# Performance work log

Measured on AMD Instinct MI355X. Metric: run time of the kernel, lower is better.

## Reference

```python
import jax, jax.numpy as jnp
import numpy as np

B, T_Q, T_K, H = 16, 1024, 1024, 1024


def _linear_params(key, fan_in, fan_out):
    kw, kb = jax.random.split(key)
    bound = 1.0 / np.sqrt(fan_in)
    W = jax.random.uniform(kw, (fan_out, fan_in), jnp.float32, -bound, bound)
    b = jax.random.uniform(kb, (fan_out,), jnp.float32, -bound, bound)
    return W, b


def setup_inputs() -> dict:
    key = jax.random.key(0)
    ks = jax.random.split(key, 6)
    query = jax.random.normal(ks[0], (B, T_Q, H), jnp.float32)
    keys = jax.random.normal(ks[1], (B, T_K, H), jnp.float32)
    values = jax.random.normal(ks[2], (B, T_K, H), jnp.float32)
    Wq, bq = _linear_params(ks[3], H, H)
    Wk, bk = _linear_params(ks[4], H, H)
    Wo, bo = _linear_params(ks[5], H, H)
    return {"query": query, "keys": keys, "values": values,
            "Wq": Wq, "bq": bq, "Wk": Wk, "bk": bk, "Wo": Wo, "bo": bo}


def reference(query, keys, values, Wq, bq, Wk, bk, Wo, bo):
    # Linear projections (torch Linear: x @ W.T + b)
    q = jnp.einsum('bth,oh->bto', query, Wq) + bq   # (B, T_Q, H)
    k = jnp.einsum('bsh,oh->bso', keys, Wk) + bk    # (B, T_K, H)
    # Unscaled scores -> softmax over key axis (dropout is identity at eval)
    scores = jnp.einsum('bto,bso->bts', q, k)       # (B, T_Q, T_K)
    attn = jax.nn.softmax(scores, axis=-1)
    ctx = jnp.einsum('bts,bsh->bth', attn, values)  # note: raw values, value_fc unused in source
    ctx = ctx / jnp.sqrt(jnp.float32(values.shape[1]))
    out = jnp.einsum('bth,oh->bto', ctx, Wo) + bo
    return out
```

## Files before the change

kernel.cpp:

```cpp
#include <hip/hip_runtime.h>
#include <math.h>

typedef __attribute__((ext_vector_type(4))) float f32x4;
typedef __attribute__((ext_vector_type(8))) _Float16 h16x8;
typedef __attribute__((ext_vector_type(8))) short s16x8;
typedef __attribute__((ext_vector_type(4))) short s16x4;

__device__ inline unsigned short f2h(float f) {
    union { _Float16 h; unsigned short u; } v; v.h = (_Float16)f; return v.u;
}
__device__ inline float h2f(unsigned short u) {
    union { unsigned short u; _Float16 h; } v; v.u = u; return (float)v.h;
}

__device__ inline void async16(const void* g, void* l) {
    __builtin_amdgcn_global_load_lds(
        (const __attribute__((address_space(1))) unsigned int*)g,
        (__attribute__((address_space(3))) unsigned int*)l, 16, 0, 0);
}

#define BM 256
#define BN 256
#define BK 64
#define NTHREADS 512


__device__ inline void stage_half(const unsigned short* g, int row0, int kel, int pitch,
                                  unsigned ldsbase, char* smem, int tid) {
    const int rl  = tid >> 3;
    const int scb = ((tid & 7) ^ (rl & 7)) << 4;
    char* wb = smem + ldsbase + (unsigned)((tid >> 6) << 10);
#pragma unroll
    for (int s = 0; s < 2; ++s) {
        long off = ((long)(row0 + s * 64 + rl) * pitch + kel) * 2 + scb;
        async16((const char*)g + off, wb + s * 8192);
    }
}

__device__ inline h16x8 ld_frag(const char* smem, unsigned base, int row, int kbyte) {
    unsigned off = base + (unsigned)(row * 128) + (unsigned)(kbyte ^ ((row & 7) << 4));
    return *(const h16x8*)(smem + off);
}

__device__ inline void xcd_swizzle(int& bx, int& by, int& bz) {
    const long gx = gridDim.x, gy = gridDim.y;
    const long nwg = gx * gy * (long)gridDim.z;
    const long hw  = ((long)blockIdx.z * gy + blockIdx.y) * gx + blockIdx.x;
    const long qq = nwg >> 3, rr = nwg & 7;
    const long xcd = hw & 7, pos = hw >> 3;
    const long lg = (xcd < rr) ? xcd * (qq + 1) + pos
                               : rr * (qq + 1) + (xcd - rr) * qq + pos;
    bx = (int)(lg % gx);
    const long rem = lg / gx;
    by = (int)(rem % gy);
    bz = (int)(rem / gy);
}

template<int OM>
__global__ __launch_bounds__(NTHREADS, 2)
void gemm256(const unsigned short* __restrict__ A,
             const unsigned short* __restrict__ B,
             const float* __restrict__ bias,
             void* __restrict__ C, int N, int lenK, int pitch,
             long sA, long sB, long sC, long sBias, float scale)
{
    __shared__ __align__(16) char smem[131072];

    const int tid  = threadIdx.x;
    const int wv   = tid >> 6;
    const int lane = tid & 63;
    const int wr = wv >> 2, wc = wv & 3;
    const int lrow = lane & 15;
    const int kq16 = (lane >> 4) * 16;

    int bx, by, bz; xcd_swizzle(bx, by, bz);
    const int n0 = bx * BN;
    const int m0 = by * BM;

    const unsigned short* Ag = A + (long)bz * sA;
    const unsigned short* Bg = B + (long)bz * sB;
    const int NT = lenK / BK;

    auto stageA = [&](int t, int h) {
        stage_half(Ag, m0 + h * 128, t * BK, pitch,
                   (unsigned)(((t & 1) << 16) + (h << 14)), smem, tid);
    };
    auto stageB = [&](int t, int h) {
        stage_half(Bg, n0 + h * 128, t * BK, pitch,
                   (unsigned)(((t & 1) << 16) + 32768 + (h << 14)), smem, tid);
    };

    f32x4 acc[8][4];
#pragma unroll
    for (int i = 0; i < 8; ++i)
#pragma unroll
        for (int j = 0; j < 4; ++j) acc[i][j] = (f32x4){0.f, 0.f, 0.f, 0.f};

    const unsigned AbaseW = (unsigned)(wr * 16384);
    const unsigned BbaseW = (unsigned)(32768 + (wc >> 1) * 16384);
    const int brow0 = (wc & 1) * 64;

    stageB(0, 0); stageB(0, 1); stageA(0, 0); stageA(0, 1); stageB(1, 0); stageB(1, 1);
    asm volatile("s_waitcnt vmcnt(4)" ::: "memory");
    __builtin_amdgcn_s_barrier();

    h16x8 bfr[4][2], afr[2][2];

    for (int i = 0; i < NT / 2; ++i) {
        const int t1 = 2 * i + 1, t2 = 2 * i + 2, t3 = 2 * i + 3;
#pragma unroll
        for (int half = 0; half < 2; ++half) {
            const unsigned hb = half ? 65536u : 0u;
#pragma unroll
            for (int q = 0; q < 4; ++q) {
                if (q == 0) {
#pragma unroll
                    for (int j = 0; j < 4; ++j)
#pragma unroll
                        for (int ks = 0; ks < 2; ++ks)
                            bfr[j][ks] = ld_frag(smem, hb + BbaseW, brow0 + j * 16 + lrow, ks * 64 + kq16);
                }
#pragma unroll
                for (int f = 0; f < 2; ++f)
#pragma unroll
                    for (int ks = 0; ks < 2; ++ks)
                        afr[f][ks] = ld_frag(smem, hb + AbaseW, q * 32 + f * 16 + lrow, ks * 64 + kq16);
                if (half == 0) {
                    if (q == 0)      stageA(t1, 0);
                    else if (q == 1) stageA(t1, 1);
                    else if (q == 2) { if (t2 < NT) stageB(t2, 0); }
                    else             { if (t2 < NT) stageB(t2, 1); }
                } else {
                    if (q == 0)      { if (t2 < NT) stageA(t2, 0); }
                    else if (q == 1) { if (t2 < NT) stageA(t2, 1); }
                    else if (q == 2) { if (t3 < NT) stageB(t3, 0); }
                    else             { if (t3 < NT) stageB(t3, 1); }
                }

                __builtin_amdgcn_s_barrier();
                asm volatile("s_waitcnt lgkmcnt(0)" ::: "memory");
                __builtin_amdgcn_sched_barrier(0);
                __builtin_amdgcn_s_setprio(1);
#pragma unroll
                for (int ks = 0; ks < 2; ++ks)
#pragma unroll
                    for (int f = 0; f < 2; ++f)
#pragma unroll
                        for (int j = 0; j < 4; ++j)
                            acc[2 * q + f][j] = __builtin_amdgcn_mfma_f32_16x16x32_f16(
                                afr[f][ks], bfr[j][ks], acc[2 * q + f][j], 0, 0, 0);
                __builtin_amdgcn_s_setprio(0);
                if (q == 3) {
                    const int tn = half ? t3 : t2;
                    if (tn < NT) { asm volatile("s_waitcnt vmcnt(4)" ::: "memory"); }
                    else         { asm volatile("s_waitcnt vmcnt(0)" ::: "memory"); }
                }
                __builtin_amdgcn_s_barrier();
            }
        }
    }

#pragma unroll
    for (int j = 0; j < 4; ++j) {
        const int col = n0 + wc * 64 + j * 16 + lrow;
        const float bb = bias ? bias[(long)bz * sBias + col] : 0.f;
#pragma unroll
        for (int mi = 0; mi < 8; ++mi) {
#pragma unroll
            for (int r = 0; r < 4; ++r) {
                const long row = m0 + wr * 128 + mi * 16 + (lane >> 4) * 4 + r;
                const float v = acc[mi][j][r] * scale + bb;
                const long idx = (long)bz * sC + row * (long)N + col;
                if constexpr (OM == 0) ((float*)C)[idx] = v;
                else                   ((unsigned short*)C)[idx] = f2h(v);
            }
        }
    }
}

__global__ __launch_bounds__(256)
void conv_f16(const float* __restrict__ in, unsigned short* __restrict__ out, int n)
{
    int i = (blockIdx.x * 256 + threadIdx.x) * 4;
    if (i >= n) return;
    float4 v = *(const float4*)(in + i);
    s16x4 o = {(short)f2h(v.x), (short)f2h(v.y), (short)f2h(v.z), (short)f2h(v.w)};
    *(s16x4*)(out + i) = o;
}

__global__ __launch_bounds__(256)
void transpose_f16(const float* __restrict__ in, unsigned short* __restrict__ out)
{
    __shared__ float tile[32][33];
    const long base = (long)blockIdx.z * 1024 * 1024;
    const int h0 = blockIdx.x * 32, t0 = blockIdx.y * 32;
    for (int i = threadIdx.y; i < 32; i += 8)
        tile[i][threadIdx.x] = in[base + (long)(t0 + i) * 1024 + h0 + threadIdx.x];
    __syncthreads();
    for (int i = threadIdx.y; i < 32; i += 8)
        out[base + (long)(h0 + i) * 1024 + t0 + threadIdx.x] = f2h(tile[threadIdx.x][i]);
}

__global__ __launch_bounds__(256)
void w2_kernel(const float* __restrict__ Wk, const float* __restrict__ bq,
               float* __restrict__ w2)
{
    __shared__ float part[4][64];
    const int tx = threadIdx.x & 63;
    const int ty = threadIdx.x >> 6;
    const int h  = blockIdx.x * 64 + tx;
    float s = 0.f;
    for (int o = ty * 256; o < ty * 256 + 256; ++o)
        s = fmaf(Wk[(long)o * 1024 + h], bq[o], s);
    part[ty][tx] = s;
    __syncthreads();
    if (ty == 0) w2[h] = part[0][tx] + part[1][tx] + part[2][tx] + part[3][tx];
}

__global__ __launch_bounds__(256)
void matvec_v(const unsigned short* __restrict__ Xk, const float* __restrict__ w2,
              float* __restrict__ v)
{
    const int wave = threadIdx.x >> 6, lane = threadIdx.x & 63;
    const long row = (long)blockIdx.x * 4 + wave;
    const unsigned short* p = Xk + row * 1024 + lane * 16;
    float s = 0.f;
#pragma unroll
    for (int c = 0; c < 2; ++c) {
        s16x8 hv = *(const s16x8*)(p + c * 8);
#pragma unroll
        for (int e = 0; e < 8; ++e)
            s = fmaf(h2f((unsigned short)hv[e]), w2[lane * 16 + c * 8 + e], s);
    }
#pragma unroll
    for (int off = 1; off < 64; off <<= 1) s += __shfl_xor(s, off);
    if (lane == 0) v[row] = s;
}

__global__ __launch_bounds__(256)
void reduce4(const float* __restrict__ p, unsigned short* __restrict__ MT)
{
    const long i = ((long)blockIdx.x * 256 + threadIdx.x) * 4;
    const long S = 1024L * 1024;
    float4 a = *(const float4*)(p + i);
    float4 b = *(const float4*)(p + S + i);
    float4 c = *(const float4*)(p + 2 * S + i);
    float4 d = *(const float4*)(p + 3 * S + i);
    s16x4 o = {(short)f2h(a.x + b.x + c.x + d.x), (short)f2h(a.y + b.y + c.y + d.y),
               (short)f2h(a.z + b.z + c.z + d.z), (short)f2h(a.w + b.w + c.w + d.w)};
    *(s16x4*)(MT + i) = o;
}

__global__ __launch_bounds__(256)
void softmax_ip(unsigned short* __restrict__ S)
{
    long row = blockIdx.x;
    const int tid = threadIdx.x;
    s16x4 raw = *(s16x4*)(S + row * 1024 + tid * 4);
    float v0 = h2f((unsigned short)raw[0]), v1 = h2f((unsigned short)raw[1]);
    float v2 = h2f((unsigned short)raw[2]), v3 = h2f((unsigned short)raw[3]);
    float m = fmaxf(fmaxf(v0, v1), fmaxf(v2, v3));
#pragma unroll
    for (int off = 1; off < 64; off <<= 1) m = fmaxf(m, __shfl_xor(m, off));
    __shared__ float redm[4];
    int wave = tid >> 6, lane = tid & 63;
    if (lane == 0) redm[wave] = m;
    __syncthreads();
    m = fmaxf(fmaxf(redm[0], redm[1]), fmaxf(redm[2], redm[3]));

    float e0 = expf(v0 - m), e1 = expf(v1 - m), e2 = expf(v2 - m), e3 = expf(v3 - m);
    float s = e0 + e1 + e2 + e3;
#pragma unroll
    for (int off = 1; off < 64; off <<= 1) s += __shfl_xor(s, off);
    __shared__ float reds[4];
    if (lane == 0) reds[wave] = s;
    __syncthreads();
    s = reds[0] + reds[1] + reds[2] + reds[3];
    float inv = 1.f / s;
    s16x4 o = {(short)f2h(e0 * inv), (short)f2h(e1 * inv),
               (short)f2h(e2 * inv), (short)f2h(e3 * inv)};
    *(s16x4*)(S + row * 1024 + tid * 4) = o;
}

extern "C" void kernel_launch(void* const* d_in, const int* in_sizes, int n_in,
                              void* d_out, int out_size, void* d_ws, size_t ws_size,
                              hipStream_t stream)
{
    const float* query  = (const float*)d_in[0];
    const float* keys   = (const float*)d_in[1];
    const float* values = (const float*)d_in[2];
    const float* Wq     = (const float*)d_in[3];
    const float* bq     = (const float*)d_in[4];
    const float* Wk     = (const float*)d_in[5];
    const float* bk     = (const float*)d_in[6];
    const float* Wo     = (const float*)d_in[7];
    const float* bo     = (const float*)d_in[8];
    (void)bk;

    const int  T = 1024, H = 1024;
    const long NE = 16384L * 1024;
    const long NW = 1024L * 1024;

    size_t need = (size_t)(NE * 4 + NW * 12 + 40960) * sizeof(unsigned short);
    if (ws_size < need) return;

    unsigned short* ws   = (unsigned short*)d_ws;
    unsigned short* Xq   = ws;
    unsigned short* Xk   = Xq + NE;
    unsigned short* vT   = Xk + NE;
    unsigned short* P1   = vT + NE;
    unsigned short* WqT  = P1 + NE;
    unsigned short* WkT  = WqT + NW;
    unsigned short* Woh  = WkT + NW;
    unsigned short* MT   = Woh + NW;
    float*          part = (float*)(MT + NW);
    float*          w2   = (float*)(MT + NW * 9);
    float*          vvec = w2 + 1024;
    unsigned short* sc   = Xq;
    unsigned short* ctx  = P1;

    conv_f16<<<16384, 256, 0, stream>>>(query, Xq, (int)NE);
    conv_f16<<<16384, 256, 0, stream>>>(keys,  Xk, (int)NE);
    transpose_f16<<<dim3(32, 32, 1), dim3(32, 8), 0, stream>>>(Wq, WqT);
    transpose_f16<<<dim3(32, 32, 1), dim3(32, 8), 0, stream>>>(Wk, WkT);
    conv_f16<<<1024, 256, 0, stream>>>(Wo, Woh, (int)NW);
    transpose_f16<<<dim3(32, 32, 16), dim3(32, 8), 0, stream>>>(values, vT);
    w2_kernel<<<16, 256, 0, stream>>>(Wk, bq, w2);

    gemm256<0><<<dim3(4, 4, 4), NTHREADS, 0, stream>>>(
        WkT, WqT, nullptr, part, 1024, 256, 1024, 256, 256, (long)NW, 0, 1.f);
    reduce4<<<1024, 256, 0, stream>>>(part, MT);

    gemm256<1><<<dim3(4, 64, 1), NTHREADS, 0, stream>>>(
        Xq, MT, nullptr, P1, H, H, H, 0, 0, 0, 0, 1.f);

    matvec_v<<<4096, 256, 0, stream>>>(Xk, w2, vvec);

    gemm256<1><<<dim3(4, 4, 16), NTHREADS, 0, stream>>>(
        P1, Xk, vvec, sc, T, H, H,
        (long)T * H, (long)T * H, (long)T * T, (long)T, 1.f);

    softmax_ip<<<16384, 256, 0, stream>>>(sc);

    gemm256<1><<<dim3(4, 4, 16), NTHREADS, 0, stream>>>(
        sc, vT, nullptr, ctx, H, T, T,
        (long)T * T, (long)T * H, (long)T * H, 0, 1.f / 32.f);

    gemm256<0><<<dim3(4, 64, 1), NTHREADS, 0, stream>>>(
        ctx, Woh, bo, d_out, H, H, H, 0, 0, 0, 0, 1.f);
}
```

Measured before the change: 306.6 us.

## Add smaller-tile GEMM for projection matmuls and merge prep kernels

Adds a 128x256 tile GEMM with BK=32, 48KB LDS and launch bounds allowing higher occupancy. It replaces the 256x256 kernel for the M precompute, the Q projection and the output projection, which doubles the workgroup count on those 1024-wide GEMMs for better CU fill. It also merges the paired conversion and transpose launches into single launches. The trade-off is less data reuse per tile and more barriers per unit of K.

```diff
diff --git a/kernel.cpp b/kernel.cpp
--- a/kernel.cpp
+++ b/kernel.cpp
@@ -17,29 +17,6 @@
     __builtin_amdgcn_global_load_lds(
         (const __attribute__((address_space(1))) unsigned int*)g,
         (__attribute__((address_space(3))) unsigned int*)l, 16, 0, 0);
-}
-
-#define BM 256
-#define BN 256
-#define BK 64
-#define NTHREADS 512
-
-
-__device__ inline void stage_half(const unsigned short* g, int row0, int kel, int pitch,
-                                  unsigned ldsbase, char* smem, int tid) {
-    const int rl  = tid >> 3;
-    const int scb = ((tid & 7) ^ (rl & 7)) << 4;
-    char* wb = smem + ldsbase + (unsigned)((tid >> 6) << 10);
-#pragma unroll
-    for (int s = 0; s < 2; ++s) {
-        long off = ((long)(row0 + s * 64 + rl) * pitch + kel) * 2 + scb;
-        async16((const char*)g + off, wb + s * 8192);
-    }
-}
-
-__device__ inline h16x8 ld_frag(const char* smem, unsigned base, int row, int kbyte) {
-    unsigned off = base + (unsigned)(row * 128) + (unsigned)(kbyte ^ ((row & 7) << 4));
-    return *(const h16x8*)(smem + off);
 }
 
 __device__ inline void xcd_swizzle(int& bx, int& by, int& bz) {
@@ -54,6 +31,28 @@
     const long rem = lg / gx;
     by = (int)(rem % gy);
     bz = (int)(rem / gy);
+}
+
+#define BM 256
+#define BN 256
+#define BK 64
+#define NTHREADS 512
+
+__device__ inline void stage_half(const unsigned short* g, int row0, int kel, int pitch,
+                                  unsigned ldsbase, char* smem, int tid) {
+    const int rl  = tid >> 3;
+    const int scb = ((tid & 7) ^ (rl & 7)) << 4;
+    char* wb = smem + ldsbase + (unsigned)((tid >> 6) << 10);
+#pragma unroll
+    for (int s = 0; s < 2; ++s) {
+        long off = ((long)(row0 + s * 64 + rl) * pitch + kel) * 2 + scb;
+        async16((const char*)g + off, wb + s * 8192);
+    }
+}
+
+__device__ inline h16x8 ld_frag(const char* smem, unsigned base, int row, int kbyte) {
+    unsigned off = base + (unsigned)(row * 128) + (unsigned)(kbyte ^ ((row & 7) << 4));
+    return *(const h16x8*)(smem + off);
 }
 
 template<int OM>
@@ -178,6 +177,119 @@
     }
 }
 
+#define BM2 128
+#define BN2 256
+#define BK2 32
+
+__device__ inline h16x8 ld_frag32(const char* smem, unsigned base, int row, int kbyte) {
+    unsigned off = base + (unsigned)(row * 64) + (unsigned)(kbyte ^ ((row & 3) << 4));
+    return *(const h16x8*)(smem + off);
+}
+
+template<int OM>
+__global__ __launch_bounds__(512, 4)
+void gemm128(const unsigned short* __restrict__ A,
+             const unsigned short* __restrict__ B,
+             const float* __restrict__ bias,
+             void* __restrict__ C, int N, int lenK, int pitch,
+             long sA, long sB, long sC, long sBias, float scale)
+{
+    __shared__ __align__(16) char smem[49152];
+
+    const int tid  = threadIdx.x;
+    const int wv   = tid >> 6;
+    const int lane = tid & 63;
+    const int wr = wv >> 2, wc = wv & 3;
+    const int lrow = lane & 15;
+    const int kq16 = (lane >> 4) * 16;
+
+    int bx, by, bz; xcd_swizzle(bx, by, bz);
+    const int n0 = bx * BN2;
+    const int m0 = by * BM2;
+
+    const unsigned short* Ag = A + (long)bz * sA;
+    const unsigned short* Bg = B + (long)bz * sB;
+    const int NT = lenK / BK2;
+
+    auto stage = [&](int t) {
+        const unsigned db = (unsigned)((t & 1) * 24576);
+        {
+            int r = tid >> 2, s = tid & 3, ss = s ^ (r & 3);
+            async16((const char*)Ag + ((long)(m0 + r) * pitch + t * BK2 + ss * 8) * 2,
+                    smem + db + (unsigned)(wv << 10));
+        }
+#pragma unroll
+        for (int l = 0; l < 2; ++l) {
+            int idx = l * 512 + tid;
+            int r = idx >> 2, s = idx & 3, ss = s ^ (r & 3);
+            async16((const char*)Bg + ((long)(n0 + r) * pitch + t * BK2 + ss * 8) * 2,
+                    smem + db + 8192u + (unsigned)(l * 8192) + (unsigned)(wv << 10));
+        }
+    };
+
+    f32x4 acc[4][4];
+#pragma unroll
+    for (int i = 0; i < 4; ++i)
+#pragma unroll
+        for (int j = 0; j < 4; ++j) acc[i][j] = (f32x4){0.f, 0.f, 0.f, 0.f};
+
+    const unsigned Abase = (unsigned)(wr * 4096);
+    const unsigned Bbase = 8192u + (unsigned)(wc * 4096);
+
+    stage(0);
+    __syncthreads();
+
+#pragma unroll 2
+    for (int t = 0; t < NT; ++t) {
+        const unsigned db = (unsigned)((t & 1) * 24576);
+        if (t + 1 < NT) stage(t + 1);
+        h16x8 afr[4], bfr[4];
+#pragma unroll
+        for (int f = 0; f < 4; ++f) {
+            afr[f] = ld_frag32(smem, db + Abase, f * 16 + lrow, kq16);
+            bfr[f] = ld_frag32(smem, db + Bbase, f * 16 + lrow, kq16);
+        }
+#pragma unroll
+        for (int mi = 0; mi < 4; ++mi)
+#pragma unroll
+            for (int j = 0; j < 4; ++j)
+                acc[mi][j] = __builtin_amdgcn_mfma_f32_16x16x32_f16(
+                    afr[mi], bfr[j], acc[mi][j], 0, 0, 0);
+        __syncthreads();
+    }
+
+#pragma unroll
+    for (int j = 0; j < 4; ++j) {
+        const int col = n0 + wc * 64 + j * 16 + lrow;
+        const float bb = bias ? bias[(long)bz * sBias + col] : 0.f;
+#pragma unroll
+        for (int mi = 0; mi < 4; ++mi) {
+#pragma unroll
+            for (int r = 0; r < 4; ++r) {
+                const long row = m0 + wr * 64 + mi * 16 + (lane >> 4) * 4 + r;
+                const float v = acc[mi][j][r] * scale + bb;
+                const long idx = (long)bz * sC + row * (long)N + col;
+                if constexpr (OM == 0) ((float*)C)[idx] = v;
+                else                   ((unsigned short*)C)[idx] = f2h(v);
+            }
+        }
+    }
+}
+
+
+__global__ __launch_bounds__(256)
+void conv2_f16(const float* __restrict__ a, const float* __restrict__ b,
+               unsigned short* __restrict__ oa, unsigned short* __restrict__ ob, int n)
+{
+    int i = (blockIdx.x * 256 + threadIdx.x) * 4;
+    if (i >= n) return;
+    const float* in = blockIdx.y ? b : a;
+    unsigned short* out = blockIdx.y ? ob : oa;
+    float4 v = *(const float4*)(in + i);
+    s16x4 o = {(short)f2h(v.x), (short)f2h(v.y), (short)f2h(v.z), (short)f2h(v.w)};
+    *(s16x4*)(out + i) = o;
+}
+
 __global__ __launch_bounds__(256)
 void conv_f16(const float* __restrict__ in, unsigned short* __restrict__ out, int n)
 {
@@ -199,6 +311,21 @@
     __syncthreads();
     for (int i = threadIdx.y; i < 32; i += 8)
         out[base + (long)(h0 + i) * 1024 + t0 + threadIdx.x] = f2h(tile[threadIdx.x][i]);
+}
+
+__global__ __launch_bounds__(256)
+void transpose2_f16(const float* __restrict__ inA, const float* __restrict__ inB,
+                    unsigned short* __restrict__ outA, unsigned short* __restrict__ outB)
+{
+    __shared__ float tile[32][33];
+    const float* in = blockIdx.z ? inB : inA;
+    unsigned short* out = blockIdx.z ? outB : outA;
+    const int h0 = blockIdx.x * 32, t0 = blockIdx.y * 32;
+    for (int i = threadIdx.y; i < 32; i += 8)
+        tile[i][threadIdx.x] = in[(long)(t0 + i) * 1024 + h0 + threadIdx.x];
+    __syncthreads();
+    for (int i = threadIdx.y; i < 32; i += 8)
+        out[(long)(h0 + i) * 1024 + t0 + threadIdx.x] = f2h(tile[threadIdx.x][i]);
 }
 
 __global__ __launch_bounds__(256)
@@ -319,19 +446,17 @@
     unsigned short* sc   = Xq;
     unsigned short* ctx  = P1;
 
-    conv_f16<<<16384, 256, 0, stream>>>(query, Xq, (int)NE);
-    conv_f16<<<16384, 256, 0, stream>>>(keys,  Xk, (int)NE);
-    transpose_f16<<<dim3(32, 32, 1), dim3(32, 8), 0, stream>>>(Wq, WqT);
-    transpose_f16<<<dim3(32, 32, 1), dim3(32, 8), 0, stream>>>(Wk, WkT);
+    conv2_f16<<<dim3(16384, 2, 1), 256, 0, stream>>>(query, keys, Xq, Xk, (int)NE);
+    transpose2_f16<<<dim3(32, 32, 2), dim3(32, 8), 0, stream>>>(Wq, Wk, WqT, WkT);
     conv_f16<<<1024, 256, 0, stream>>>(Wo, Woh, (int)NW);
     transpose_f16<<<dim3(32, 32, 16), dim3(32, 8), 0, stream>>>(values, vT);
     w2_kernel<<<16, 256, 0, stream>>>(Wk, bq, w2);
 
-    gemm256<0><<<dim3(4, 4, 4), NTHREADS, 0, stream>>>(
+    gemm128<0><<<dim3(4, 8, 4), 512, 0, stream>>>(
         WkT, WqT, nullptr, part, 1024, 256, 1024, 256, 256, (long)NW, 0, 1.f);
     reduce4<<<1024, 256, 0, stream>>>(part, MT);
 
-    gemm256<1><<<dim3(4, 64, 1), NTHREADS, 0, stream>>>(
+    gemm128<1><<<dim3(4, 128, 1), 512, 0, stream>>>(
         Xq, MT, nullptr, P1, H, H, H, 0, 0, 0, 0, 1.f);
 
     matvec_v<<<4096, 256, 0, stream>>>(Xk, w2, vvec);
@@ -346,6 +471,6 @@
         sc, vT, nullptr, ctx, H, T, T,
         (long)T * T, (long)T * H, (long)T * H, 0, 1.f / 32.f);
 
-    gemm256<0><<<dim3(4, 64, 1), NTHREADS, 0, stream>>>(
+    gemm128<0><<<dim3(4, 128, 1), 512, 0, stream>>>(
         ctx, Woh, bo, d_out, H, H, H, 0, 0, 0, 0, 1.f);
 }
```

New measurement: 300.1 us. 2.1% less time.
